# Kernel tuning notes

Measured on AMD Instinct MI355X. Metric: run time of the kernel, lower is better.

Reference implementation:

```python
import jax, jax.numpy as jnp
import numpy as np
import math

EMBED = 1024
HEADS = 16
HEAD_DIM = EMBED // HEADS
B, S = 4, 2048
FF = 4 * EMBED
EPS = 1e-5


def _layernorm(x, g, b):
    mu = jnp.mean(x, axis=-1, keepdims=True)
    var = jnp.mean(jnp.square(x - mu), axis=-1, keepdims=True)
    return (x - mu) * jax.lax.rsqrt(var + EPS) * g + b


def setup_inputs() -> dict:
    key = jax.random.key(0)
    ks = jax.random.split(key, 12)
    sd_e = 1.0 / math.sqrt(EMBED)
    sd_ff = 1.0 / math.sqrt(FF)
    return {
        "x": jax.random.normal(ks[0], (B, S, EMBED), jnp.float32),
        # attention weights stored [in, out] (transposed torch Linear)
        "Wq": jax.random.normal(ks[1], (EMBED, EMBED), jnp.float32) * sd_e,
        "bq": jnp.zeros((EMBED,), jnp.float32),
        "Wk": jax.random.normal(ks[2], (EMBED, EMBED), jnp.float32) * sd_e,
        "bk": jnp.zeros((EMBED,), jnp.float32),
        "Wv": jax.random.normal(ks[3], (EMBED, EMBED), jnp.float32) * sd_e,
        "bv": jnp.zeros((EMBED,), jnp.float32),
        "Wo": jax.random.normal(ks[4], (EMBED, EMBED), jnp.float32) * sd_e,
        "bo": jnp.zeros((EMBED,), jnp.float32),
        "g1": jnp.ones((EMBED,), jnp.float32),
        "beta1": jnp.zeros((EMBED,), jnp.float32),
        "g2": jnp.ones((EMBED,), jnp.float32),
        "beta2": jnp.zeros((EMBED,), jnp.float32),
        "W1": jax.random.normal(ks[5], (EMBED, FF), jnp.float32) * sd_e,
        "b1": jnp.zeros((FF,), jnp.float32),
        "W2": jax.random.normal(ks[6], (FF, EMBED), jnp.float32) * sd_ff,
        "b2": jnp.zeros((EMBED,), jnp.float32),
    }


def reference(x, Wq, bq, Wk, bk, Wv, bv, Wo, bo, g1, beta1, g2, beta2, W1, b1, W2, b2):
    b, s, _ = x.shape
    # --- pre-LN causal self-attention (dropout in eval = identity) ---
    h = _layernorm(x, g1, beta1)
    q = (h @ Wq + bq).reshape(b, s, HEADS, HEAD_DIM)
    k = (h @ Wk + bk).reshape(b, s, HEADS, HEAD_DIM)
    v = (h @ Wv + bv).reshape(b, s, HEADS, HEAD_DIM)
    scores = jnp.einsum("bqhd,bkhd->bhqk", q, k) / math.sqrt(HEAD_DIM)
    causal = jnp.tril(jnp.ones((s, s), bool))
    scores = jnp.where(causal, scores, jnp.float32(-1e8))
    attn = jax.nn.softmax(scores, axis=-1)
    y = jnp.einsum("bhqk,bkhd->bqhd", attn, v).reshape(b, s, EMBED)
    x = x + (y @ Wo + bo)
    # --- GELU MLP (exact erf gelu, torch default) ---
    h2 = _layernorm(x, g2, beta2)
    ff = jax.nn.gelu(h2 @ W1 + b1, approximate=False) @ W2 + b2
    return x + ff
```

## Files before the change

kernel.cpp:

```cpp
#include <hip/hip_runtime.h>
#include <hip/hip_bf16.h>
#include <stdint.h>
#include <math.h>

#define SEQ 2048
#define NTOK 8192
#define EMB 1024
#define NH 16
#define HD 64
#define FFD 4096

using us = unsigned short;
using b8 = __attribute__((ext_vector_type(8))) __bf16;
using f4 = __attribute__((ext_vector_type(4))) float;

__device__ __forceinline__ us f2b(float f) {
  union { float f; uint32_t u; } v; v.f = f;
  uint32_t u = v.u;
  return (us)((u + 0x7fffu + ((u >> 16) & 1u)) >> 16);
}

__device__ __forceinline__ uint32_t pkbf(float a, float b) {
  union { float f; uint32_t u; } x, y; x.f = a; y.f = b;
  return ((x.u + 0x8000u) >> 16) | ((y.u + 0x8000u) & 0xFFFF0000u);
}

__device__ __forceinline__ void async16(void* lds, const void* g) {
  __builtin_amdgcn_global_load_lds(
      (__attribute__((address_space(1))) void*)(uintptr_t)g,
      (__attribute__((address_space(3))) void*)(uintptr_t)lds, 16, 0, 0);
}

__device__ __forceinline__ float gelu_f(float x) {
  const float z = -2.30211416f * x * (1.f + 0.044715f * x * x);
  return x / (1.f + __builtin_amdgcn_exp2f(z));
}

__global__ __launch_bounds__(256)
void transpose_cast(const float* __restrict__ in, us* __restrict__ out, int R, int C) {
  __shared__ float tile[32][33];
  const int bc = blockIdx.x * 32, br = blockIdx.y * 32;
  const int tx = threadIdx.x & 31, ty = threadIdx.x >> 5;
#pragma unroll
  for (int i = 0; i < 32; i += 8)
    tile[ty + i][tx] = in[(size_t)(br + ty + i) * C + bc + tx];
  __syncthreads();
#pragma unroll
  for (int i = 0; i < 32; i += 8)
    out[(size_t)(bc + ty + i) * R + br + tx] = f2b(tile[tx][ty + i]);
}

__global__ void pack_bias(const float* __restrict__ bq, const float* __restrict__ bk,
                          const float* __restrict__ bv, float* __restrict__ o) {
  int i = blockIdx.x * 256 + threadIdx.x;
  o[i] = (i < 1024) ? bq[i] : (i < 2048 ? bk[i - 1024] : bv[i - 2048]);
}

__global__ __launch_bounds__(256)
void ln_kernel(const float* __restrict__ x, const float* __restrict__ g,
               const float* __restrict__ be, us* __restrict__ out) {
  __shared__ float red[8];
  const int row = blockIdx.x, t = threadIdx.x;
  const float4 v = ((const float4*)(x + (size_t)row * EMB))[t];
  float s = v.x + v.y + v.z + v.w;
  float s2 = v.x * v.x + v.y * v.y + v.z * v.z + v.w * v.w;
#pragma unroll
  for (int o = 32; o; o >>= 1) { s += __shfl_down(s, o, 64); s2 += __shfl_down(s2, o, 64); }
  if ((t & 63) == 0) { red[(t >> 6) * 2] = s; red[(t >> 6) * 2 + 1] = s2; }
  __syncthreads();
  const float ts = red[0] + red[2] + red[4] + red[6];
  const float ts2 = red[1] + red[3] + red[5] + red[7];
  const float mu = ts * (1.f / 1024.f);
  const float rs = rsqrtf(ts2 * (1.f / 1024.f) - mu * mu + 1e-5f);
  const float4 gv = ((const float4*)g)[t];
  const float4 bv = ((const float4*)be)[t];
  ushort4 o4;
  o4.x = f2b((v.x - mu) * rs * gv.x + bv.x);
  o4.y = f2b((v.y - mu) * rs * gv.y + bv.y);
  o4.z = f2b((v.z - mu) * rs * gv.z + bv.z);
  o4.w = f2b((v.w - mu) * rs * gv.w + bv.w);
  ((ushort4*)(out + (size_t)row * EMB))[t] = o4;
}

__global__ __launch_bounds__(256, 3)
void gemm_bt(const us* __restrict__ A, const us* __restrict__ Bt,
             const float* __restrict__ bias, const float* __restrict__ resid,
             float* __restrict__ outF, us* __restrict__ outB,
             int M, int N, int K, int gelu) {
  __shared__ us As[2 * 128 * 32];
  __shared__ us Bs[2 * 128 * 32];
  const int tid = threadIdx.x;
  const int wave = tid >> 6, lane = tid & 63;
  const int wm = wave & 1, wn = wave >> 1;
  const int quad = lane >> 4, l15 = lane & 15;
  const int row0 = blockIdx.x * 128, col0 = blockIdx.y * 128;

  const f4 zf = {0.f, 0.f, 0.f, 0.f};
  f4 acc[4][4];
#pragma unroll
  for (int i = 0; i < 4; i++)
#pragma unroll
    for (int j = 0; j < 4; j++) acc[i][j] = zf;

  const int srow = lane >> 2;
  const int scol = (lane & 3) * 8;
  const us* Ap = A + (size_t)(row0 + wave * 32 + srow) * K + scol;
  const us* Bp = Bt + (size_t)(col0 + wave * 32 + srow) * K + scol;
  us* asb = &As[(wave * 32) * 32];
  us* bsb = &Bs[(wave * 32) * 32];
  const size_t rstep = (size_t)16 * K;

  for (int k0 = 0; k0 < K; k0 += 64) {
#pragma unroll
    for (int s = 0; s < 2; s++) {
      const int kc = k0 + s * 32;
      async16(asb + s * 4096, Ap + kc);
      async16(asb + s * 4096 + 512, Ap + rstep + kc);
      async16(bsb + s * 4096, Bp + kc);
      async16(bsb + s * 4096 + 512, Bp + rstep + kc);
    }
    __syncthreads();
#pragma unroll
    for (int s = 0; s < 2; s++) {
      b8 af[4], bf[4];
#pragma unroll
      for (int i = 0; i < 4; i++) {
        af[i] = *(const b8*)&As[s * 4096 + (wm * 64 + i * 16 + l15) * 32 + quad * 8];
        bf[i] = *(const b8*)&Bs[s * 4096 + (wn * 64 + i * 16 + l15) * 32 + quad * 8];
      }
#pragma unroll
      for (int i = 0; i < 4; i++)
#pragma unroll
        for (int j = 0; j < 4; j++)
          acc[i][j] = __builtin_amdgcn_mfma_f32_16x16x32_bf16(af[i], bf[j], acc[i][j], 0, 0, 0);
    }
    __syncthreads();
  }

  float bcol[4];
#pragma unroll
  for (int j = 0; j < 4; j++) bcol[j] = bias[col0 + wn * 64 + j * 16 + l15];
#pragma unroll
  for (int i = 0; i < 4; i++)
#pragma unroll
    for (int j = 0; j < 4; j++)
#pragma unroll
      for (int r = 0; r < 4; r++) {
        const int grow = row0 + wm * 64 + i * 16 + quad * 4 + r;
        const int gcol = col0 + wn * 64 + j * 16 + l15;
        float v = acc[i][j][r] + bcol[j];
        if (resid) v += resid[(size_t)grow * N + gcol];
        if (gelu) v = gelu_f(v);
        if (outF) outF[(size_t)grow * N + gcol] = v;
        if (outB) outB[(size_t)grow * N + gcol] = f2b(v);
      }
}

__global__ __launch_bounds__(256, 4)
void gemm_bt64(const us* __restrict__ A, const us* __restrict__ Bt,
               const float* __restrict__ bias, const float* __restrict__ resid,
               float* __restrict__ outF, us* __restrict__ outB,
               int M, int N, int K, int gelu) {
  __shared__ us As[2 * 64 * 32];
  __shared__ us Bs[2 * 128 * 32];
  const int tid = threadIdx.x;
  const int wave = tid >> 6, lane = tid & 63;
  const int quad = lane >> 4, l15 = lane & 15;
  const int row0 = blockIdx.x * 64, col0 = blockIdx.y * 128;

  const f4 zf = {0.f, 0.f, 0.f, 0.f};
  f4 acc[4][2];
#pragma unroll
  for (int i = 0; i < 4; i++) { acc[i][0] = zf; acc[i][1] = zf; }

  const int srow = lane >> 2;
  const int scol = (lane & 3) * 8;
  const us* Ap = A + (size_t)(row0 + wave * 16 + srow) * K + scol;
  const us* Bp = Bt + (size_t)(col0 + wave * 32 + srow) * K + scol;
  us* asb = &As[(wave * 16) * 32];
  us* bsb = &Bs[(wave * 32) * 32];
  const size_t rstep = (size_t)16 * K;

  for (int k0 = 0; k0 < K; k0 += 64) {
#pragma unroll
    for (int s = 0; s < 2; s++) {
      const int kc = k0 + s * 32;
      async16(asb + s * 2048, Ap + kc);
      async16(bsb + s * 4096, Bp + kc);
      async16(bsb + s * 4096 + 512, Bp + rstep + kc);
    }
    __syncthreads();
#pragma unroll
    for (int s = 0; s < 2; s++) {
      b8 af[4], bf[2];
#pragma unroll
      for (int i = 0; i < 4; i++)
        af[i] = *(const b8*)&As[s * 2048 + (i * 16 + l15) * 32 + quad * 8];
#pragma unroll
      for (int j = 0; j < 2; j++)
        bf[j] = *(const b8*)&Bs[s * 4096 + (wave * 32 + j * 16 + l15) * 32 + quad * 8];
#pragma unroll
      for (int i = 0; i < 4; i++)
#pragma unroll
        for (int j = 0; j < 2; j++)
          acc[i][j] = __builtin_amdgcn_mfma_f32_16x16x32_bf16(af[i], bf[j], acc[i][j], 0, 0, 0);
    }
    __syncthreads();
  }

  float bcol[2];
#pragma unroll
  for (int j = 0; j < 2; j++) bcol[j] = bias[col0 + wave * 32 + j * 16 + l15];
#pragma unroll
  for (int i = 0; i < 4; i++)
#pragma unroll
    for (int j = 0; j < 2; j++)
#pragma unroll
      for (int r = 0; r < 4; r++) {
        const int grow = row0 + i * 16 + quad * 4 + r;
        const int gcol = col0 + wave * 32 + j * 16 + l15;
        float v = acc[i][j][r] + bcol[j];
        if (resid) v += resid[(size_t)grow * N + gcol];
        if (gelu) v = gelu_f(v);
        if (outF) outF[(size_t)grow * N + gcol] = v;
        if (outB) outB[(size_t)grow * N + gcol] = f2b(v);
      }
}

__global__ __launch_bounds__(256, 3)
void attn(const us* __restrict__ qkv, us* __restrict__ y) {
  static const signed char QTM[16] = {15,14,13,12, 10,11,8,9, 5,4,7,6, 0,1,2,3};
  const int bx = blockIdx.x;
  const int bh = bx & 63;
  const int qt = QTM[(bx >> 6) & 15];
  const int bb = bh >> 4, h = bh & 15;
  const int tid = threadIdx.x;
  const int wave = tid >> 6, lane = tid & 63;
  const int quad = lane >> 4, l15 = lane & 15;

  __shared__ us Ks[128 * 64];
  __shared__ us Vt[64 * 132];

  const size_t base = (size_t)bb * SEQ * 3072;
  const int q0 = qt * 128;

  b8 bqf[2][2];
#pragma unroll
  for (int qg = 0; qg < 2; qg++) {
    const us* qp = qkv + base + (size_t)(q0 + wave * 32 + qg * 16 + l15) * 3072 + h * 64 + quad * 8;
    bqf[qg][0] = *(const b8*)qp;
    bqf[qg][1] = *(const b8*)(qp + 32);
  }

  const f4 zf = {0.f, 0.f, 0.f, 0.f};
  f4 o[2][4];
  float mrow[2], lrow[2];
#pragma unroll
  for (int qg = 0; qg < 2; qg++) {
    mrow[qg] = -3.0e38f; lrow[qg] = 0.f;
#pragma unroll
    for (int dg = 0; dg < 4; dg++) o[qg][dg] = zf;
  }

  const int klr = lane >> 3, klc = lane & 7;
  const us* kgbase = qkv + base + (size_t)(wave * 32 + klr) * 3072 + 1024 + h * 64 + ((klc ^ klr) << 3);
  const us* vgbase = qkv + base + (size_t)(2 * lane) * 3072 + 2048 + h * 64 + wave * 8;

  const float sm_scale = 0.125f * 1.44269504088896340736f;

  for (int kt = 0; kt <= qt; kt++) {
    const size_t koff = (size_t)kt * 128 * 3072;
#pragma unroll
    for (int op = 0; op < 4; op++)
      async16(&Ks[(wave * 32 + op * 8) * 64], kgbase + koff + (size_t)op * 8 * 3072);
    {
      union { float4 f; us u[8]; } v0, v1, v2, v3;
      v0.f = *(const float4*)(vgbase + koff);
      v1.f = *(const float4*)(vgbase + koff + 3072);
      v2.f = *(const float4*)(vgbase + koff + 32);
      v3.f = *(const float4*)(vgbase + koff + 3072 + 32);
#pragma unroll
      for (int j = 0; j < 8; j++) {
        *(uint32_t*)&Vt[(wave * 8 + j) * 132 + 2 * lane] =
            (uint32_t)v0.u[j] | ((uint32_t)v1.u[j] << 16);
        *(uint32_t*)&Vt[(32 + wave * 8 + j) * 132 + 2 * lane] =
            (uint32_t)v2.u[j] | ((uint32_t)v3.u[j] << 16);
      }
    }
    __syncthreads();

    f4 sacc[2][8];
#pragma unroll
    for (int c = 0; c < 8; c++) {
      const int krow = (c * 16 + l15) * 64;
      const int sw = l15 & 7;
      const b8 ak0 = *(const b8*)&Ks[krow + ((quad ^ sw) << 3)];
      const b8 ak1 = *(const b8*)&Ks[krow + (((quad ^ 4) ^ sw) << 3)];
#pragma unroll
      for (int qg = 0; qg < 2; qg++) {
        f4 s = __builtin_amdgcn_mfma_f32_16x16x32_bf16(ak0, bqf[qg][0], zf, 0, 0, 0);
        sacc[qg][c] = __builtin_amdgcn_mfma_f32_16x16x32_bf16(ak1, bqf[qg][1], s, 0, 0, 0);
      }
    }

    uint32_t pf[2][16];
    float alpha[2];
#pragma unroll
    for (int qg = 0; qg < 2; qg++) {
      const int q_in = wave * 32 + qg * 16 + l15;
#pragma unroll
      for (int c = 0; c < 8; c++)
#pragma unroll
        for (int r = 0; r < 4; r++) {
          float v = sacc[qg][c][r] * sm_scale;
          if (kt == qt && (c * 16 + quad * 4 + r) > q_in) v = -3.0e38f;
          sacc[qg][c][r] = v;
        }
      float mx = sacc[qg][0][0];
#pragma unroll
      for (int c = 0; c < 8; c++)
#pragma unroll
        for (int r = 0; r < 4; r++) mx = fmaxf(mx, sacc[qg][c][r]);
      mx = fmaxf(mx, __shfl_xor(mx, 16, 64));
      mx = fmaxf(mx, __shfl_xor(mx, 32, 64));
      const float mnew = fmaxf(mrow[qg], mx);
      alpha[qg] = __builtin_amdgcn_exp2f(mrow[qg] - mnew);
      mrow[qg] = mnew;
      float rs = 0.f;
#pragma unroll
      for (int c = 0; c < 8; c++) {
        const float p0 = __builtin_amdgcn_exp2f(sacc[qg][c][0] - mnew);
        const float p1 = __builtin_amdgcn_exp2f(sacc[qg][c][1] - mnew);
        const float p2 = __builtin_amdgcn_exp2f(sacc[qg][c][2] - mnew);
        const float p3 = __builtin_amdgcn_exp2f(sacc[qg][c][3] - mnew);
        rs += (p0 + p1) + (p2 + p3);
        pf[qg][c * 2] = pkbf(p0, p1);
        pf[qg][c * 2 + 1] = pkbf(p2, p3);
      }
      rs += __shfl_xor(rs, 16, 64);
      rs += __shfl_xor(rs, 32, 64);
      lrow[qg] = lrow[qg] * alpha[qg] + rs;
#pragma unroll
      for (int r = 0; r < 4; r++) {
        const float ar = __shfl(alpha[qg], quad * 4 + r, 64);
#pragma unroll
        for (int dg = 0; dg < 4; dg++) o[qg][dg][r] *= ar;
      }
    }

#pragma unroll
    for (int c = 0; c < 8; c++) {
      union { uint32_t w[4]; b8 v; } af0, af1;
      af0.w[0] = pf[0][c * 2]; af0.w[1] = pf[0][c * 2 + 1]; af0.w[2] = 0u; af0.w[3] = 0u;
      af1.w[0] = pf[1][c * 2]; af1.w[1] = pf[1][c * 2 + 1]; af1.w[2] = 0u; af1.w[3] = 0u;
#pragma unroll
      for (int dg = 0; dg < 4; dg++) {
        const uint2 vd = *(const uint2*)&Vt[(dg * 16 + l15) * 132 + c * 16 + quad * 4];
        union { uint32_t w[4]; b8 v; } vb;
        vb.w[0] = vd.x; vb.w[1] = vd.y; vb.w[2] = 0u; vb.w[3] = 0u;
        o[0][dg] = __builtin_amdgcn_mfma_f32_16x16x32_bf16(af0.v, vb.v, o[0][dg], 0, 0, 0);
        o[1][dg] = __builtin_amdgcn_mfma_f32_16x16x32_bf16(af1.v, vb.v, o[1][dg], 0, 0, 0);
      }
    }
    __syncthreads();
  }

#pragma unroll
  for (int qg = 0; qg < 2; qg++) {
    float lr[4];
#pragma unroll
    for (int r = 0; r < 4; r++) lr[r] = __shfl(lrow[qg], quad * 4 + r, 64);
#pragma unroll
    for (int dg = 0; dg < 4; dg++)
#pragma unroll
      for (int r = 0; r < 4; r++) {
        const int gq = q0 + wave * 32 + qg * 16 + quad * 4 + r;
        y[(size_t)(bb * SEQ + gq) * EMB + h * 64 + dg * 16 + l15] = f2b(o[qg][dg][r] / lr[r]);
      }
  }
}

extern "C" void kernel_launch(void* const* d_in, const int* in_sizes, int n_in,
                              void* d_out, int out_size, void* d_ws, size_t ws_size,
                              hipStream_t stream) {
  const float* x = (const float*)d_in[0];
  const float* Wq = (const float*)d_in[1];
  const float* bq = (const float*)d_in[2];
  const float* Wk = (const float*)d_in[3];
  const float* bk = (const float*)d_in[4];
  const float* Wv = (const float*)d_in[5];
  const float* bv = (const float*)d_in[6];
  const float* Wo = (const float*)d_in[7];
  const float* bo = (const float*)d_in[8];
  const float* g1 = (const float*)d_in[9];
  const float* be1 = (const float*)d_in[10];
  const float* g2 = (const float*)d_in[11];
  const float* be2 = (const float*)d_in[12];
  const float* W1 = (const float*)d_in[13];
  const float* b1 = (const float*)d_in[14];
  const float* W2 = (const float*)d_in[15];
  const float* b2 = (const float*)d_in[16];
  float* out = (float*)d_out;

  char* ws = (char*)d_ws;
  const size_t MB = 1024ull * 1024ull;
  us* WqkvT = (us*)(ws + 0);
  us* WoT   = (us*)(ws + 6 * MB);
  us* W1T   = (us*)(ws + 8 * MB);
  us* W2T   = (us*)(ws + 16 * MB);
  us* hbuf  = (us*)(ws + 24 * MB);
  us* qkvb  = (us*)(ws + 40 * MB);
  us* ybuf  = (us*)(ws + 88 * MB);
  float* x1 = (float*)(ws + 104 * MB);
  us* h2    = (us*)(ws + 136 * MB);
  us* ff1   = (us*)(ws + 24 * MB);
  float* bqkv = (float*)(ws + 152 * MB);

  transpose_cast<<<dim3(32, 32), 256, 0, stream>>>(Wq, WqkvT, 1024, 1024);
  transpose_cast<<<dim3(32, 32), 256, 0, stream>>>(Wk, WqkvT + 1024 * 1024, 1024, 1024);
  transpose_cast<<<dim3(32, 32), 256, 0, stream>>>(Wv, WqkvT + 2 * 1024 * 1024, 1024, 1024);
  transpose_cast<<<dim3(32, 32), 256, 0, stream>>>(Wo, WoT, 1024, 1024);
  transpose_cast<<<dim3(128, 32), 256, 0, stream>>>(W1, W1T, 1024, 4096);
  transpose_cast<<<dim3(32, 128), 256, 0, stream>>>(W2, W2T, 4096, 1024);
  pack_bias<<<12, 256, 0, stream>>>(bq, bk, bv, bqkv);

  ln_kernel<<<NTOK, 256, 0, stream>>>(x, g1, be1, hbuf);
  gemm_bt<<<dim3(64, 24), 256, 0, stream>>>(hbuf, WqkvT, bqkv, nullptr, nullptr, qkvb,
                                            NTOK, 3072, 1024, 0);
  attn<<<1024, 256, 0, stream>>>(qkvb, ybuf);
  gemm_bt64<<<dim3(128, 8), 256, 0, stream>>>(ybuf, WoT, bo, x, x1, nullptr,
                                              NTOK, 1024, 1024, 0);
  ln_kernel<<<NTOK, 256, 0, stream>>>(x1, g2, be2, h2);
  gemm_bt<<<dim3(64, 32), 256, 0, stream>>>(h2, W1T, b1, nullptr, nullptr, ff1,
                                            NTOK, 4096, 1024, 1);
  gemm_bt64<<<dim3(128, 8), 256, 0, stream>>>(ff1, W2T, b2, x1, out, nullptr,
                                              NTOK, 1024, 4096, 0);
}
```

Baseline: 559.6 us.

## Replace GEMM kernels with 8-wave 256-row tiles, swizzled LDS and deeper prefetch

Both bf16 GEMM kernels are replaced by one templated 512-thread kernel. It computes 256xBN output tiles with K-step 64, XOR-swizzled LDS layout, and double-buffered async global-to-LDS loads kept one stage ahead using explicit vmcnt waits. It also remaps block IDs across XCDs and raises wave priority around the MFMA bursts. The larger tiles are meant to increase operand reuse and cut global traffic and barriers. In exchange, LDS use and register pressure are much higher, occupancy drops to about one block per CU, and the smaller N=1024 GEMMs launch only 256 blocks.

```diff
diff --git a/kernel.cpp b/kernel.cpp
--- a/kernel.cpp
+++ b/kernel.cpp
@@ -30,6 +30,9 @@
       (__attribute__((address_space(1))) void*)(uintptr_t)g,
       (__attribute__((address_space(3))) void*)(uintptr_t)lds, 16, 0, 0);
 }
+
+#define FENCED_BARRIER() do { asm volatile("" ::: "memory"); \
+  __builtin_amdgcn_s_barrier(); asm volatile("" ::: "memory"); } while (0)
 
 __device__ __forceinline__ float gelu_f(float x) {
   const float z = -2.30211416f * x * (1.f + 0.044715f * x * x);
@@ -82,149 +85,118 @@
   ((ushort4*)(out + (size_t)row * EMB))[t] = o4;
 }
 
-__global__ __launch_bounds__(256, 3)
-void gemm_bt(const us* __restrict__ A, const us* __restrict__ Bt,
-             const float* __restrict__ bias, const float* __restrict__ resid,
-             float* __restrict__ outF, us* __restrict__ outB,
-             int M, int N, int K, int gelu) {
-  __shared__ us As[2 * 128 * 32];
-  __shared__ us Bs[2 * 128 * 32];
-  const int tid = threadIdx.x;
-  const int wave = tid >> 6, lane = tid & 63;
-  const int wm = wave & 1, wn = wave >> 1;
+template<int BN>
+__global__ __launch_bounds__(512, 2)
+void gemm8(const us* __restrict__ A, const us* __restrict__ Bt,
+           const float* __restrict__ bias, const float* __restrict__ resid,
+           float* __restrict__ outF, us* __restrict__ outB,
+           int M, int N, int K, int gelu, int gy) {
+  constexpr int NF = BN / 64;
+  constexpr int BROWS = BN / 8;
+  constexpr int BINSTS = BN / 64;
+  __shared__ us As[2][256 * 64];
+  __shared__ us Bs[2][BN * 64];
+
+  int bid = blockIdx.x;
+  const int cpx = (int)gridDim.x >> 3;
+  bid = (bid & 7) * cpx + (bid >> 3);
+  const int bx = bid / gy, by = bid - bx * gy;
+  const int row0 = bx * 256, col0 = by * BN;
+
+  const int tid = threadIdx.x, w = tid >> 6, lane = tid & 63;
+  const int wm = w >> 2, wn = w & 3;
   const int quad = lane >> 4, l15 = lane & 15;
-  const int row0 = blockIdx.x * 128, col0 = blockIdx.y * 128;
+
+  const int srow = lane >> 3;
+  const int soct = (lane & 7) ^ srow;
+  const us* Ag = A + (size_t)(row0 + w * 32 + srow) * K + soct * 8;
+  const us* Bg = Bt + (size_t)(col0 + w * BROWS + srow) * K + soct * 8;
+  const int NT = K >> 6;
 
   const f4 zf = {0.f, 0.f, 0.f, 0.f};
-  f4 acc[4][4];
-#pragma unroll
-  for (int i = 0; i < 4; i++)
-#pragma unroll
-    for (int j = 0; j < 4; j++) acc[i][j] = zf;
-
-  const int srow = lane >> 2;
-  const int scol = (lane & 3) * 8;
-  const us* Ap = A + (size_t)(row0 + wave * 32 + srow) * K + scol;
-  const us* Bp = Bt + (size_t)(col0 + wave * 32 + srow) * K + scol;
-  us* asb = &As[(wave * 32) * 32];
-  us* bsb = &Bs[(wave * 32) * 32];
-  const size_t rstep = (size_t)16 * K;
-
-  for (int k0 = 0; k0 < K; k0 += 64) {
-#pragma unroll
-    for (int s = 0; s < 2; s++) {
-      const int kc = k0 + s * 32;
-      async16(asb + s * 4096, Ap + kc);
-      async16(asb + s * 4096 + 512, Ap + rstep + kc);
-      async16(bsb + s * 4096, Bp + kc);
-      async16(bsb + s * 4096 + 512, Bp + rstep + kc);
-    }
-    __syncthreads();
-#pragma unroll
-    for (int s = 0; s < 2; s++) {
-      b8 af[4], bf[4];
-#pragma unroll
-      for (int i = 0; i < 4; i++) {
-        af[i] = *(const b8*)&As[s * 4096 + (wm * 64 + i * 16 + l15) * 32 + quad * 8];
-        bf[i] = *(const b8*)&Bs[s * 4096 + (wn * 64 + i * 16 + l15) * 32 + quad * 8];
-      }
-#pragma unroll
-      for (int i = 0; i < 4; i++)
-#pragma unroll
-        for (int j = 0; j < 4; j++)
-          acc[i][j] = __builtin_amdgcn_mfma_f32_16x16x32_bf16(af[i], bf[j], acc[i][j], 0, 0, 0);
-    }
-    __syncthreads();
-  }
-
-  float bcol[4];
-#pragma unroll
-  for (int j = 0; j < 4; j++) bcol[j] = bias[col0 + wn * 64 + j * 16 + l15];
-#pragma unroll
-  for (int i = 0; i < 4; i++)
-#pragma unroll
-    for (int j = 0; j < 4; j++)
+  f4 acc[8][NF];
+#pragma unroll
+  for (int i = 0; i < 8; i++)
+#pragma unroll
+    for (int j = 0; j < NF; j++) acc[i][j] = zf;
+
+  auto STAGE = [&](int buf, int t) {
+    const size_t ko = (size_t)t * 64;
+#pragma unroll
+    for (int i = 0; i < 4; i++)
+      async16(&As[buf][(w * 32 + i * 8) * 64], Ag + ko + (size_t)(i * 8) * K);
+#pragma unroll
+    for (int i = 0; i < BINSTS; i++)
+      async16(&Bs[buf][(w * BROWS + i * 8) * 64], Bg + ko + (size_t)(i * 8) * K);
+  };
+
+  STAGE(0, 0);
+  STAGE(1, 1);
+  if constexpr (BN == 256) asm volatile("s_waitcnt vmcnt(8)" ::: "memory");
+  else                     asm volatile("s_waitcnt vmcnt(6)" ::: "memory");
+  FENCED_BARRIER();
+
+  const int xr = l15 & 7;
+  for (int u = 0; u < NT; u++) {
+    const int cb = u & 1;
+    const us* __restrict__ as = As[cb];
+    const us* __restrict__ bs = Bs[cb];
+    b8 bf[2][NF];
+#pragma unroll
+    for (int s = 0; s < 2; s++)
+#pragma unroll
+      for (int nf = 0; nf < NF; nf++)
+        bf[s][nf] = *(const b8*)&bs[(wn * (NF * 16) + nf * 16 + l15) * 64 +
+                                    ((((s << 2) + quad) ^ xr) << 3)];
+#pragma unroll
+    for (int qm = 0; qm < 2; qm++) {
+      b8 af[2][4];
+#pragma unroll
+      for (int s = 0; s < 2; s++)
+#pragma unroll
+        for (int mi = 0; mi < 4; mi++)
+          af[s][mi] = *(const b8*)&as[(wm * 128 + qm * 64 + mi * 16 + l15) * 64 +
+                                      ((((s << 2) + quad) ^ xr) << 3)];
+      __builtin_amdgcn_s_setprio(1);
+#pragma unroll
+      for (int s = 0; s < 2; s++)
+#pragma unroll
+        for (int mi = 0; mi < 4; mi++)
+#pragma unroll
+          for (int nf = 0; nf < NF; nf++)
+            acc[qm * 4 + mi][nf] = __builtin_amdgcn_mfma_f32_16x16x32_bf16(
+                af[s][mi], bf[s][nf], acc[qm * 4 + mi][nf], 0, 0, 0);
+      __builtin_amdgcn_s_setprio(0);
+    }
+    asm volatile("s_waitcnt lgkmcnt(0)" ::: "memory");
+    FENCED_BARRIER();
+    if (u + 2 < NT) {
+      STAGE(cb, u + 2);
+      if constexpr (BN == 256) asm volatile("s_waitcnt vmcnt(8)" ::: "memory");
+      else                     asm volatile("s_waitcnt vmcnt(6)" ::: "memory");
+    } else {
+      asm volatile("s_waitcnt vmcnt(0)" ::: "memory");
+    }
+    if (u + 1 < NT) FENCED_BARRIER();
+  }
+
+#pragma unroll
+  for (int mi8 = 0; mi8 < 8; mi8++) {
+#pragma unroll
+    for (int nf = 0; nf < NF; nf++) {
+      const int gcol = col0 + wn * (NF * 16) + nf * 16 + l15;
+      const float bc = bias[gcol];
 #pragma unroll
       for (int r = 0; r < 4; r++) {
-        const int grow = row0 + wm * 64 + i * 16 + quad * 4 + r;
-        const int gcol = col0 + wn * 64 + j * 16 + l15;
-        float v = acc[i][j][r] + bcol[j];
+        const int grow = row0 + wm * 128 + mi8 * 16 + quad * 4 + r;
+        float v = acc[mi8][nf][r] + bc;
         if (resid) v += resid[(size_t)grow * N + gcol];
         if (gelu) v = gelu_f(v);
         if (outF) outF[(size_t)grow * N + gcol] = v;
         if (outB) outB[(size_t)grow * N + gcol] = f2b(v);
       }
-}
-
-__global__ __launch_bounds__(256, 4)
-void gemm_bt64(const us* __restrict__ A, const us* __restrict__ Bt,
-               const float* __restrict__ bias, const float* __restrict__ resid,
-               float* __restrict__ outF, us* __restrict__ outB,
-               int M, int N, int K, int gelu) {
-  __shared__ us As[2 * 64 * 32];
-  __shared__ us Bs[2 * 128 * 32];
-  const int tid = threadIdx.x;
-  const int wave = tid >> 6, lane = tid & 63;
-  const int quad = lane >> 4, l15 = lane & 15;
-  const int row0 = blockIdx.x * 64, col0 = blockIdx.y * 128;
-
-  const f4 zf = {0.f, 0.f, 0.f, 0.f};
-  f4 acc[4][2];
-#pragma unroll
-  for (int i = 0; i < 4; i++) { acc[i][0] = zf; acc[i][1] = zf; }
-
-  const int srow = lane >> 2;
-  const int scol = (lane & 3) * 8;
-  const us* Ap = A + (size_t)(row0 + wave * 16 + srow) * K + scol;
-  const us* Bp = Bt + (size_t)(col0 + wave * 32 + srow) * K + scol;
-  us* asb = &As[(wave * 16) * 32];
-  us* bsb = &Bs[(wave * 32) * 32];
-  const size_t rstep = (size_t)16 * K;
-
-  for (int k0 = 0; k0 < K; k0 += 64) {
-#pragma unroll
-    for (int s = 0; s < 2; s++) {
-      const int kc = k0 + s * 32;
-      async16(asb + s * 2048, Ap + kc);
-      async16(bsb + s * 4096, Bp + kc);
-      async16(bsb + s * 4096 + 512, Bp + rstep + kc);
-    }
-    __syncthreads();
-#pragma unroll
-    for (int s = 0; s < 2; s++) {
-      b8 af[4], bf[2];
-#pragma unroll
-      for (int i = 0; i < 4; i++)
-        af[i] = *(const b8*)&As[s * 2048 + (i * 16 + l15) * 32 + quad * 8];
-#pragma unroll
-      for (int j = 0; j < 2; j++)
-        bf[j] = *(const b8*)&Bs[s * 4096 + (wave * 32 + j * 16 + l15) * 32 + quad * 8];
-#pragma unroll
-      for (int i = 0; i < 4; i++)
-#pragma unroll
-        for (int j = 0; j < 2; j++)
-          acc[i][j] = __builtin_amdgcn_mfma_f32_16x16x32_bf16(af[i], bf[j], acc[i][j], 0, 0, 0);
-    }
-    __syncthreads();
-  }
-
-  float bcol[2];
-#pragma unroll
-  for (int j = 0; j < 2; j++) bcol[j] = bias[col0 + wave * 32 + j * 16 + l15];
-#pragma unroll
-  for (int i = 0; i < 4; i++)
-#pragma unroll
-    for (int j = 0; j < 2; j++)
-#pragma unroll
-      for (int r = 0; r < 4; r++) {
-        const int grow = row0 + i * 16 + quad * 4 + r;
-        const int gcol = col0 + wave * 32 + j * 16 + l15;
-        float v = acc[i][j][r] + bcol[j];
-        if (resid) v += resid[(size_t)grow * N + gcol];
-        if (gelu) v = gelu_f(v);
-        if (outF) outF[(size_t)grow * N + gcol] = v;
-        if (outB) outB[(size_t)grow * N + gcol] = f2b(v);
-      }
+    }
+  }
 }
 
 __global__ __launch_bounds__(256, 3)
@@ -425,14 +397,14 @@
   pack_bias<<<12, 256, 0, stream>>>(bq, bk, bv, bqkv);
 
   ln_kernel<<<NTOK, 256, 0, stream>>>(x, g1, be1, hbuf);
-  gemm_bt<<<dim3(64, 24), 256, 0, stream>>>(hbuf, WqkvT, bqkv, nullptr, nullptr, qkvb,
-                                            NTOK, 3072, 1024, 0);
+  gemm8<128><<<dim3(32 * 24), 512, 0, stream>>>(hbuf, WqkvT, bqkv, nullptr, nullptr, qkvb,
+                                                NTOK, 3072, 1024, 0, 24);
   attn<<<1024, 256, 0, stream>>>(qkvb, ybuf);
-  gemm_bt64<<<dim3(128, 8), 256, 0, stream>>>(ybuf, WoT, bo, x, x1, nullptr,
-                                              NTOK, 1024, 1024, 0);
+  gemm8<128><<<dim3(32 * 8), 512, 0, stream>>>(ybuf, WoT, bo, x, x1, nullptr,
+                                               NTOK, 1024, 1024, 0, 8);
   ln_kernel<<<NTOK, 256, 0, stream>>>(x1, g2, be2, h2);
-  gemm_bt<<<dim3(64, 32), 256, 0, stream>>>(h2, W1T, b1, nullptr, nullptr, ff1,
-                                            NTOK, 4096, 1024, 1);
-  gemm_bt64<<<dim3(128, 8), 256, 0, stream>>>(ff1, W2T, b2, x1, out, nullptr,
-                                              NTOK, 1024, 4096, 0);
-}
+  gemm8<256><<<dim3(32 * 16), 512, 0, stream>>>(h2, W1T, b1, nullptr, nullptr, ff1,
+                                                NTOK, 4096, 1024, 1, 16);
+  gemm8<128><<<dim3(32 * 8), 512, 0, stream>>>(ff1, W2T, b2, x1, out, nullptr,
+                                               NTOK, 1024, 4096, 0, 8);
+}
```

Result: no change. 570.8 us (+2.0%).
